# Kernel optimization log

Hardware: AMD Instinct MI355X
Metric: run time of the kernel (lower is better)

The kernel has to match this reference:

```python
import jax, jax.numpy as jnp
import numpy as np

B, TXT_T, MEL_T, N_MEL = 32, 256, 1600, 40
PAD_MAG = 1.0e12


def setup_inputs() -> dict:
    key = jax.random.key(0)
    k1, k2, k3, k4 = jax.random.split(key, 4)
    mu_logvar = jax.random.normal(k1, (B, TXT_T, 2 * N_MEL), jnp.float32)
    z = jax.random.normal(k2, (B, N_MEL, MEL_T), jnp.float32)
    text_lengths = jax.random.randint(k3, (B,), TXT_T // 2, TXT_T + 1).astype(jnp.int32)
    mel_lengths = jax.random.randint(k4, (B,), MEL_T // 2, MEL_T + 1).astype(jnp.int32)
    return {"mu_logvar": mu_logvar, "z": z,
            "text_lengths": text_lengths, "mel_lengths": mel_lengths}


def _mdn_log_prob(mu_logvar, z):
    # mu_logvar: [B, L, 2C], z: [B, C, T] -> log_prob_matrix [B, L, T]
    C = z.shape[1]
    mu, logvar = jnp.split(mu_logvar, 2, axis=-1)          # [B, L, C] each
    invvar = jnp.exp(-logvar)                               # [B, L, C]
    # mean_c((z - mu)^2 * invvar) expanded via matmuls (no [B,L,T,C] tensor)
    t1 = jnp.einsum('bct,blc->blt', z * z, invvar)
    t2 = jnp.einsum('bct,blc->blt', z, mu * invvar)
    t3 = jnp.sum(mu * mu * invvar, axis=-1)[:, :, None]
    mse = t1 - 2.0 * t2 + t3                                # [B, L, T]
    return -0.5 * (mse / C + jnp.mean(logvar, axis=-1)[:, :, None])


def _forward_dp(lp):
    # forward algorithm: log_alpha over (txt position, mel time) via scan over T
    Bb, L, T = lp.shape
    alpha0 = jnp.full((Bb, L + 1), -PAD_MAG, lp.dtype).at[:, 1].set(lp[:, 0, 0])

    def step(alpha, lp_t):
        stay = alpha[:, 1:] + 1e-7
        go = alpha[:, :-1] + 1e-7
        new = jnp.logaddexp(stay, go) + lp_t                # [B, L]
        alpha_new = jnp.concatenate(
            [jnp.full((Bb, 1), -PAD_MAG, lp.dtype), new], axis=1)
        return alpha_new, new

    _, ys = jax.lax.scan(step, alpha0, jnp.moveaxis(lp[:, :, 1:], 2, 0))
    log_alpha = jnp.concatenate([alpha0[:, 1:][None], ys], axis=0)  # [T, B, L]
    return log_alpha


def _viterbi(lp, text_lengths, mel_lengths):
    Bb, L, T = lp.shape
    beta0 = jnp.full((Bb, L), -PAD_MAG, lp.dtype).at[:, 0].set(lp[:, 0, 0])

    def fstep(beta, lp_t):
        shifted = jnp.concatenate(
            [jnp.full((Bb, 1), -PAD_MAG, lp.dtype), beta[:, :-1]], axis=1)
        new = jnp.maximum(beta, shifted) + lp_t
        return new, new

    _, ys = jax.lax.scan(fstep, beta0, jnp.moveaxis(lp[:, :, 1:], 2, 0))
    log_beta = jnp.transpose(jnp.concatenate([beta0[None], ys], axis=0), (1, 2, 0))  # [B, L, T]

    b_idx = jnp.arange(Bb)
    r0 = (text_lengths - 1).astype(jnp.float32)
    c0 = (mel_lengths - 1).astype(jnp.float32)

    def bstep(carry, _):
        rows, cols = carry
        ri = rows.astype(jnp.int32)
        ci = cols.astype(jnp.int32)
        # torch negative indexing wraps -> emulate with mod
        val_go = log_beta[b_idx, (ri - 1) % L, (ci - 1) % T]
        val_stay = log_beta[b_idx, ri % L, (ci - 1) % T]
        is_go = (val_go > val_stay).astype(rows.dtype)
        new_rows = jax.nn.relu(rows - is_go + 1.0) - 1.0
        new_cols = jax.nn.relu(cols) - 1.0
        return (new_rows, new_cols), new_rows

    _, path_ys = jax.lax.scan(bstep, (r0, c0), None, length=T - 1)
    full = jnp.concatenate([r0[None], path_ys], axis=0)     # [T, B], backward order
    path = full[::-1].T                                     # [B, T], chronological
    align = jax.nn.one_hot(path.astype(jnp.int32), L, dtype=lp.dtype)  # [B, T, L]

    def shift(a, ml):
        # F.pad(..., (-pad, pad)) on time axis: shift valid region to the front
        rolled = jnp.roll(a, -(T - ml), axis=0)
        mask = (jnp.arange(T) < ml)[:, None].astype(a.dtype)
        return rolled * mask

    return jax.vmap(shift)(align, mel_lengths)              # [B, T, L]


def reference(mu_logvar, z, text_lengths, mel_lengths):
    lp = _mdn_log_prob(mu_logvar, z)                        # [B, L, T]
    log_alpha = _forward_dp(lp)                             # [T, B, L]
    b_idx = jnp.arange(lp.shape[0])
    alpha_last = log_alpha[mel_lengths - 1, b_idx, text_lengths - 1]
    mdn_loss = -(alpha_last / mel_lengths.astype(alpha_last.dtype))  # [B]
    alignment = _viterbi(lp, text_lengths, mel_lengths)     # [B, T, L]
    return mdn_loss, alignment, lp
```

## Files before the change

### kernel.cpp

```cpp
#include <hip/hip_runtime.h>
#include <cstdint>
#include <math.h>

#define BB   32
#define LLEN 256
#define TLEN 1600
#define NC   40
#define NEGPADF (-1.0e12f)
#define NEGPADD (-1.0e12)

#define OFF_ALIGN 32
#define OFF_LP    (32 + (size_t)BB * TLEN * LLEN)

#define WSB_A    0
#define WSB_KC   (WSB_A + (size_t)BB * LLEN * 80 * 8)
#define WSB_LPT  (WSB_KC + (size_t)BB * LLEN * 8)
#define WSB_PATH (WSB_LPT + (size_t)BB * TLEN * LLEN * 4)

__device__ __forceinline__ int imin(int a, int b) { return a < b ? a : b; }

__device__ __forceinline__ float lsef(float a, float b) {
  a += 1e-7f; b += 1e-7f;
  float m = fmaxf(a, b);
  float d = fabsf(a - b);
  return m + __logf(1.0f + __expf(-d));
}

__global__ __launch_bounds__(256) void prep_kernel(
    const float* __restrict__ mu_logvar, double* __restrict__ A, double* __restrict__ Kc) {
  int row = blockIdx.x * 4 + (threadIdx.x >> 6);
  int lane = threadIdx.x & 63;
  const float* src = mu_logvar + (size_t)row * (2 * NC);
  double mu = 0.0, lv = 0.0, iv = 0.0, part = 0.0;
  if (lane < NC) {
    mu = (double)src[lane];
    lv = (double)src[NC + lane];
    iv = exp(-lv);
    part = mu * mu * iv + lv;
  }
  for (int m = 1; m < 64; m <<= 1) part += __shfl_xor(part, m, 64);
  const double s = -0.5 / (double)NC;
  if (lane < NC) {
    A[(size_t)row * 80 + lane]      = s * iv;
    A[(size_t)row * 80 + NC + lane] = (1.0 / (double)NC) * mu * iv;
  }
  if (lane == 0) Kc[row] = s * part;
}

__global__ __launch_bounds__(128) void lp_kernel(
    const float* __restrict__ z, const double* __restrict__ A,
    const double* __restrict__ Kc, float* __restrict__ out,
    float* __restrict__ lpTh) {
  int b  = blockIdx.z;
  int l0 = blockIdx.y * 32;
  int t0 = blockIdx.x * 128;
  int tid = threadIdx.x;
  int t = t0 + tid;
  int tv = imin(t, TLEN - 1);
  bool act = (t < TLEN);

  float* lp_out = out + OFF_LP;
  float* loS    = out + OFF_ALIGN;

  float zr[NC];
  const float* zb = z + (size_t)b * NC * TLEN;
  #pragma unroll
  for (int c = 0; c < NC; ++c) zr[c] = zb[(size_t)c * TLEN + tv];

  __shared__ __align__(16) double tile[128][33];
  const double* Ab = A + ((size_t)b * LLEN + l0) * 80;
  const double* Kb = Kc + (size_t)b * LLEN + l0;

  #pragma unroll 2
  for (int j = 0; j < 32; ++j) {
    const double* Ar = Ab + (size_t)j * 80;
    double a0 = Kb[j], a1 = 0.0, a2 = 0.0, a3 = 0.0;
    #pragma unroll
    for (int c = 0; c < NC; c += 2) {
      double z0 = (double)zr[c], z1 = (double)zr[c + 1];
      a0 = fma(Ar[c],          z0 * z0, a0);
      a1 = fma(Ar[NC + c],     z0,      a1);
      a2 = fma(Ar[c + 1],      z1 * z1, a2);
      a3 = fma(Ar[NC + c + 1], z1,      a3);
    }
    double accd = (a0 + a2) + (a1 + a3);
    if (act) lp_out[((size_t)b * LLEN + l0 + j) * TLEN + t] = (float)accd;
    tile[tid][j] = accd;
  }
  __syncthreads();
  #pragma unroll
  for (int p = 0; p < 8; ++p) {
    int idx = p * 128 + tid;
    int r = idx >> 3, c4 = idx & 7;
    int tr = t0 + r;
    if (tr < TLEN) {
      float h[4], lo[4];
      #pragma unroll
      for (int i = 0; i < 4; ++i) {
        double d = tile[r][c4 * 4 + i];
        float hh = (float)d;
        h[i] = hh;
        lo[i] = (float)(d - (double)hh);
      }
      size_t base = ((size_t)b * TLEN + tr) * LLEN + l0 + c4 * 4;
      *(float4*)(lpTh + base) = make_float4(h[0], h[1], h[2], h[3]);
      *(float4*)(loS + base)  = make_float4(lo[0], lo[1], lo[2], lo[3]);
    }
  }
}

__global__ __launch_bounds__(64) void dp_kernel(
    const float* __restrict__ lpTh, const float* __restrict__ outR,
    const int* __restrict__ tlen, const int* __restrict__ mlen,
    float* __restrict__ out, int* __restrict__ pathg) {
  int bid = blockIdx.x;
  int lane = threadIdx.x;
  bool is_beta = (bid >= BB);
  int b = is_beta ? bid - BB : bid;
  int tl = tlen[b];
  int ml = mlen[b];
  const float* lpb = lpTh + (size_t)b * TLEN * LLEN;
  const float* lob = outR + OFF_ALIGN + (size_t)b * TLEN * LLEN;
  int rsrc = (lane + 63) & 63;

  if (!is_beta) {
    float4 ring[16];
    #pragma unroll
    for (int k = 0; k < 16; ++k)
      ring[k] = *(const float4*)(lpb + (size_t)imin(1 + k, TLEN - 1) * LLEN + 4 * lane);
    float lp00 = lpb[0];
    float o0 = (lane == 0) ? lp00 : NEGPADF;
    float o1 = NEGPADF, o2 = NEGPADF, o3 = NEGPADF;
    float q = __shfl(o3, rsrc, 64);
    auto step = [&](int t, float4& slot) {
      float4 lp4 = slot;
      slot = *(const float4*)(lpb + (size_t)imin(t + 16, TLEN - 1) * LLEN + 4 * lane);
      float p = (lane == 0) ? NEGPADF : q;
      float n0 = lsef(o0, p)  + lp4.x;
      float n1 = lsef(o1, o0) + lp4.y;
      float n2 = lsef(o2, o1) + lp4.z;
      float n3 = lsef(o3, o2) + lp4.w;
      o0 = n0; o1 = n1; o2 = n2; o3 = n3;
      q = __shfl(o3, rsrc, 64);
    };
    int t = 1;
    for (; t + 15 < ml; t += 16) {
      step(t + 0,  ring[0]);  step(t + 1,  ring[1]);
      step(t + 2,  ring[2]);  step(t + 3,  ring[3]);
      step(t + 4,  ring[4]);  step(t + 5,  ring[5]);
      step(t + 6,  ring[6]);  step(t + 7,  ring[7]);
      step(t + 8,  ring[8]);  step(t + 9,  ring[9]);
      step(t + 10, ring[10]); step(t + 11, ring[11]);
      step(t + 12, ring[12]); step(t + 13, ring[13]);
      step(t + 14, ring[14]); step(t + 15, ring[15]);
    }
    #pragma unroll
    for (int k = 0; k < 16; ++k) { if (t + k < ml) step(t + k, ring[k]); }
    int fr = tl - 1;
    if (lane == (fr >> 2)) {
      int s = fr & 3;
      float val = (s == 0) ? o0 : (s == 1) ? o1 : (s == 2) ? o2 : o3;
      out[b] = -val / (float)ml;
    }
  } else {
    __shared__ uint32_t Dbits[256][TLEN / 32];
    float4 rh[16], rl[16];
    #pragma unroll
    for (int k = 0; k < 16; ++k) {
      size_t off = (size_t)imin(1 + k, TLEN - 1) * LLEN + 4 * lane;
      rh[k] = *(const float4*)(lpb + off);
      rl[k] = *(const float4*)(lob + off);
    }
    double lp00 = (double)lpb[0] + (double)lob[0];
    double o0 = (lane == 0) ? lp00 : NEGPADD;
    double o1 = NEGPADD, o2 = NEGPADD, o3 = NEGPADD;
    double q = __shfl(o3, rsrc, 64);
    uint32_t a0 = 0, a1 = (lane == 0) ? 1u : 0u, a2 = 0, a3 = 0;
    auto step = [&](int t, float4& sh, float4& sl) {
      double l0 = (double)sh.x + (double)sl.x;
      double l1 = (double)sh.y + (double)sl.y;
      double l2 = (double)sh.z + (double)sl.z;
      double l3 = (double)sh.w + (double)sl.w;
      size_t off = (size_t)imin(t + 16, TLEN - 1) * LLEN + 4 * lane;
      sh = *(const float4*)(lpb + off);
      sl = *(const float4*)(lob + off);
      double p = (lane == 0) ? NEGPADD : q;
      double n0 = fmax(o0, p)  + l0;
      double n1 = fmax(o1, o0) + l1;
      double n2 = fmax(o2, o1) + l2;
      double n3 = fmax(o3, o2) + l3;
      q = __shfl(n3, rsrc, 64);
      uint32_t bit = 1u << (t & 31);
      if (q  > n0) a0 |= bit;
      if (n0 > n1) a1 |= bit;
      if (n1 > n2) a2 |= bit;
      if (n2 > n3) a3 |= bit;
      o0 = n0; o1 = n1; o2 = n2; o3 = n3;
      if ((t & 31) == 31) {
        int w = t >> 5;
        Dbits[4 * lane + 0][w] = a0; a0 = 0;
        Dbits[4 * lane + 1][w] = a1; a1 = 0;
        Dbits[4 * lane + 2][w] = a2; a2 = 0;
        Dbits[4 * lane + 3][w] = a3; a3 = 0;
      }
    };
    int t = 1;
    for (; t + 15 < ml; t += 16) {
      step(t + 0,  rh[0],  rl[0]);  step(t + 1,  rh[1],  rl[1]);
      step(t + 2,  rh[2],  rl[2]);  step(t + 3,  rh[3],  rl[3]);
      step(t + 4,  rh[4],  rl[4]);  step(t + 5,  rh[5],  rl[5]);
      step(t + 6,  rh[6],  rl[6]);  step(t + 7,  rh[7],  rl[7]);
      step(t + 8,  rh[8],  rl[8]);  step(t + 9,  rh[9],  rl[9]);
      step(t + 10, rh[10], rl[10]); step(t + 11, rh[11], rl[11]);
      step(t + 12, rh[12], rl[12]); step(t + 13, rh[13], rl[13]);
      step(t + 14, rh[14], rl[14]); step(t + 15, rh[15], rl[15]);
    }
    #pragma unroll
    for (int k = 0; k < 16; ++k) { if (t + k < ml) step(t + k, rh[k], rl[k]); }
    if (((ml - 1) & 31) != 31) {
      int w = (ml - 1) >> 5;
      Dbits[4 * lane + 0][w] = a0;
      Dbits[4 * lane + 1][w] = a1;
      Dbits[4 * lane + 2][w] = a2;
      Dbits[4 * lane + 3][w] = a3;
    }
    __builtin_amdgcn_s_waitcnt(0xC07F);

    if (lane == 0) {
      int* pb = pathg + b * TLEN;
      int r = tl - 1;
      pb[ml - 1] = r;
      int curR = 1 << 30, curW = -1;
      uint32_t W = 0;
      for (int qq = ml - 2; qq >= 0; --qq) {
        int w = qq >> 5;
        if (r >= 0 && (r != curR || w != curW)) { W = Dbits[r][w]; curR = r; curW = w; }
        int g = (r >= 0) ? (int)((W >> (qq & 31)) & 1u) : 0;
        r -= g;
        pb[qq] = r;
      }
    }
  }
}

__global__ __launch_bounds__(256) void zero_kernel(float* __restrict__ out) {
  size_t i = ((size_t)blockIdx.x * 256 + threadIdx.x) * 4;
  *(float4*)(out + OFF_ALIGN + i) = make_float4(0.f, 0.f, 0.f, 0.f);
}

__global__ __launch_bounds__(256) void ones_kernel(
    const int* __restrict__ mlen, const int* __restrict__ pathg, float* __restrict__ out) {
  int b = blockIdx.x;
  int ml = mlen[b];
  float* al = out + OFF_ALIGN;
  for (int t = threadIdx.x; t < ml; t += 256) {
    int p = pathg[b * TLEN + t];
    if (p >= 0) al[((size_t)b * TLEN + t) * LLEN + p] = 1.0f;
  }
}

extern "C" void kernel_launch(void* const* d_in, const int* in_sizes, int n_in,
                              void* d_out, int out_size, void* d_ws, size_t ws_size,
                              hipStream_t stream) {
  const float* mu_logvar = (const float*)d_in[0];
  const float* z         = (const float*)d_in[1];
  const int*   tlv       = (const int*)d_in[2];
  const int*   mlv       = (const int*)d_in[3];
  float* out = (float*)d_out;
  char*  wsb = (char*)d_ws;

  double* Ad   = (double*)(wsb + WSB_A);
  double* Kcd  = (double*)(wsb + WSB_KC);
  float*  lpTh = (float*)(wsb + WSB_LPT);
  int*    path = (int*)(wsb + WSB_PATH);

  prep_kernel<<<dim3(BB * LLEN / 4), 256, 0, stream>>>(mu_logvar, Ad, Kcd);
  lp_kernel<<<dim3(13, 8, BB), 128, 0, stream>>>(z, Ad, Kcd, out, lpTh);
  dp_kernel<<<dim3(2 * BB), 64, 0, stream>>>(lpTh, out, tlv, mlv, out, path);
  zero_kernel<<<dim3((BB * TLEN * LLEN) / (256 * 4)), 256, 0, stream>>>(out);
  ones_kernel<<<dim3(BB), 256, 0, stream>>>(mlv, path, out);
}
```

Before: 588.8 us.

## Add producer wave staging DP inputs via double-buffered LDS; fuse zero+ones kernels

The DP kernel now runs two waves per block. A producer wave loads batches of lp rows from global memory into a double-buffered shared-memory ring and synchronizes with s_barrier, so the consumer wave's serial recurrence only reads from LDS instead of waiting on global loads. The zero-fill and one-hot scatter kernels are merged into a single finalize kernel, which removes a launch and the separate pass. The lp tile-transpose is split into two halves to shrink shared memory. The cost is a barrier on every batch of 8 steps, and the consumer now runs padded iterations past ml, which needs the captured final values and the tail handling of the Dbits words.

```diff
diff --git a/kernel.cpp b/kernel.cpp
--- a/kernel.cpp
+++ b/kernel.cpp
@@ -8,6 +8,7 @@
 #define NC   40
 #define NEGPADF (-1.0e12f)
 #define NEGPADD (-1.0e12)
+#define NBATCH 8
 
 #define OFF_ALIGN 32
 #define OFF_LP    (32 + (size_t)BB * TLEN * LLEN)
@@ -19,11 +20,18 @@
 
 __device__ __forceinline__ int imin(int a, int b) { return a < b ? a : b; }
 
-__device__ __forceinline__ float lsef(float a, float b) {
-  a += 1e-7f; b += 1e-7f;
-  float m = fmaxf(a, b);
-  float d = fabsf(a - b);
-  return m + __logf(1.0f + __expf(-d));
+#define WAIT_LGKM0 0xC07F
+
+__device__ __forceinline__ void bar_prod() {
+  asm volatile("" ::: "memory");
+  __builtin_amdgcn_s_waitcnt(WAIT_LGKM0);
+  __builtin_amdgcn_s_barrier();
+  asm volatile("" ::: "memory");
+}
+__device__ __forceinline__ void bar_cons() {
+  asm volatile("" ::: "memory");
+  __builtin_amdgcn_s_barrier();
+  asm volatile("" ::: "memory");
 }
 
 __global__ __launch_bounds__(256) void prep_kernel(
@@ -67,164 +75,186 @@
   #pragma unroll
   for (int c = 0; c < NC; ++c) zr[c] = zb[(size_t)c * TLEN + tv];
 
-  __shared__ __align__(16) double tile[128][33];
+  __shared__ __align__(16) double tile[128][17];
   const double* Ab = A + ((size_t)b * LLEN + l0) * 80;
   const double* Kb = Kc + (size_t)b * LLEN + l0;
 
-  #pragma unroll 2
-  for (int j = 0; j < 32; ++j) {
-    const double* Ar = Ab + (size_t)j * 80;
-    double a0 = Kb[j], a1 = 0.0, a2 = 0.0, a3 = 0.0;
+  for (int g = 0; g < 2; ++g) {
+    for (int j16 = 0; j16 < 16; ++j16) {
+      int j = g * 16 + j16;
+      const double* Ar = Ab + (size_t)j * 80;
+      double a0 = Kb[j], a1 = 0.0, a2 = 0.0, a3 = 0.0;
+      #pragma unroll
+      for (int c = 0; c < NC; c += 2) {
+        double z0 = (double)zr[c], z1 = (double)zr[c + 1];
+        a0 = fma(Ar[c],          z0 * z0, a0);
+        a1 = fma(Ar[NC + c],     z0,      a1);
+        a2 = fma(Ar[c + 1],      z1 * z1, a2);
+        a3 = fma(Ar[NC + c + 1], z1,      a3);
+      }
+      double accd = (a0 + a2) + (a1 + a3);
+      if (act) lp_out[((size_t)b * LLEN + l0 + j) * TLEN + t] = (float)accd;
+      tile[tid][j16] = accd;
+    }
+    __syncthreads();
     #pragma unroll
-    for (int c = 0; c < NC; c += 2) {
-      double z0 = (double)zr[c], z1 = (double)zr[c + 1];
-      a0 = fma(Ar[c],          z0 * z0, a0);
-      a1 = fma(Ar[NC + c],     z0,      a1);
-      a2 = fma(Ar[c + 1],      z1 * z1, a2);
-      a3 = fma(Ar[NC + c + 1], z1,      a3);
-    }
-    double accd = (a0 + a2) + (a1 + a3);
-    if (act) lp_out[((size_t)b * LLEN + l0 + j) * TLEN + t] = (float)accd;
-    tile[tid][j] = accd;
-  }
-  __syncthreads();
-  #pragma unroll
-  for (int p = 0; p < 8; ++p) {
-    int idx = p * 128 + tid;
-    int r = idx >> 3, c4 = idx & 7;
-    int tr = t0 + r;
-    if (tr < TLEN) {
-      float h[4], lo[4];
-      #pragma unroll
-      for (int i = 0; i < 4; ++i) {
-        double d = tile[r][c4 * 4 + i];
-        float hh = (float)d;
-        h[i] = hh;
-        lo[i] = (float)(d - (double)hh);
-      }
-      size_t base = ((size_t)b * TLEN + tr) * LLEN + l0 + c4 * 4;
-      *(float4*)(lpTh + base) = make_float4(h[0], h[1], h[2], h[3]);
-      *(float4*)(loS + base)  = make_float4(lo[0], lo[1], lo[2], lo[3]);
-    }
-  }
-}
-
-__global__ __launch_bounds__(64) void dp_kernel(
-    const float* __restrict__ lpTh, const float* __restrict__ outR,
+    for (int p = 0; p < 4; ++p) {
+      int idx = p * 128 + tid;
+      int r = idx >> 2, c4 = idx & 3;
+      int tr = t0 + r;
+      if (tr < TLEN) {
+        float h[4], lo[4];
+        #pragma unroll
+        for (int i = 0; i < 4; ++i) {
+          double d = tile[r][c4 * 4 + i];
+          float hh = (float)d;
+          h[i] = hh;
+          lo[i] = (float)(d - (double)hh);
+        }
+        size_t base = ((size_t)b * TLEN + tr) * LLEN + l0 + g * 16 + c4 * 4;
+        *(float4*)(lpTh + base) = make_float4(h[0], h[1], h[2], h[3]);
+        *(float4*)(loS + base)  = make_float4(lo[0], lo[1], lo[2], lo[3]);
+      }
+    }
+    __syncthreads();
+  }
+}
+
+__global__ __launch_bounds__(128, 1) void dp_kernel(
+    const float* __restrict__ lpTh, const float* outR,
     const int* __restrict__ tlen, const int* __restrict__ mlen,
     float* __restrict__ out, int* __restrict__ pathg) {
   int bid = blockIdx.x;
-  int lane = threadIdx.x;
   bool is_beta = (bid >= BB);
   int b = is_beta ? bid - BB : bid;
+  int tid = threadIdx.x;
+  int lane = tid & 63;
+  int wv = tid >> 6;
   int tl = tlen[b];
   int ml = mlen[b];
   const float* lpb = lpTh + (size_t)b * TLEN * LLEN;
   const float* lob = outR + OFF_ALIGN + (size_t)b * TLEN * LLEN;
-  int rsrc = (lane + 63) & 63;
-
-  if (!is_beta) {
-    float4 ring[16];
-    #pragma unroll
-    for (int k = 0; k < 16; ++k)
-      ring[k] = *(const float4*)(lpb + (size_t)imin(1 + k, TLEN - 1) * LLEN + 4 * lane);
+  int nint = (ml - 2 + NBATCH) / NBATCH;
+
+  __shared__ __align__(16) float hbuf[2][NBATCH][LLEN];
+  __shared__ __align__(16) float lbuf[2][NBATCH][LLEN];
+  __shared__ uint32_t Dbits[LLEN][TLEN / 32];
+
+  if (wv == 1) {
+    const float* ph = lpb + 4 * lane;
+    const float* pl = lob + 4 * lane;
+    float4 Ah[NBATCH], Al[NBATCH], Bh[NBATCH], Bl[NBATCH];
+    auto ld_batch = [&](int w, float4* Dh, float4* Dl) {
+      #pragma unroll
+      for (int j = 0; j < NBATCH; ++j) {
+        int c = imin(1 + NBATCH * w + j, TLEN - 1);
+        Dh[j] = *(const float4*)(ph + (size_t)c * LLEN);
+        if (is_beta) Dl[j] = *(const float4*)(pl + (size_t)c * LLEN);
+      }
+    };
+    auto st_batch = [&](int w, float4* Dh, float4* Dl) {
+      int s = w & 1;
+      #pragma unroll
+      for (int j = 0; j < NBATCH; ++j) {
+        *(float4*)(&hbuf[s][j][4 * lane]) = Dh[j];
+        if (is_beta) *(float4*)(&lbuf[s][j][4 * lane]) = Dl[j];
+      }
+    };
+    ld_batch(0, Ah, Al);
+    ld_batch(1, Bh, Bl);
+    for (int w = 0; w < nint; w += 2) {
+      st_batch(w, Ah, Al);
+      bar_prod();
+      ld_batch(w + 2, Ah, Al);
+      if (w + 1 < nint) {
+        st_batch(w + 1, Bh, Bl);
+        bar_prod();
+        ld_batch(w + 3, Bh, Bl);
+      }
+    }
+  } else if (!is_beta) {
+    int rsrc = (lane + 63) & 63;
     float lp00 = lpb[0];
     float o0 = (lane == 0) ? lp00 : NEGPADF;
     float o1 = NEGPADF, o2 = NEGPADF, o3 = NEGPADF;
+    float f0 = o0, f1 = o1, f2 = o2, f3 = o3;
     float q = __shfl(o3, rsrc, 64);
-    auto step = [&](int t, float4& slot) {
-      float4 lp4 = slot;
-      slot = *(const float4*)(lpb + (size_t)imin(t + 16, TLEN - 1) * LLEN + 4 * lane);
-      float p = (lane == 0) ? NEGPADF : q;
-      float n0 = lsef(o0, p)  + lp4.x;
-      float n1 = lsef(o1, o0) + lp4.y;
-      float n2 = lsef(o2, o1) + lp4.z;
-      float n3 = lsef(o3, o2) + lp4.w;
-      o0 = n0; o1 = n1; o2 = n2; o3 = n3;
-      q = __shfl(o3, rsrc, 64);
-    };
     int t = 1;
-    for (; t + 15 < ml; t += 16) {
-      step(t + 0,  ring[0]);  step(t + 1,  ring[1]);
-      step(t + 2,  ring[2]);  step(t + 3,  ring[3]);
-      step(t + 4,  ring[4]);  step(t + 5,  ring[5]);
-      step(t + 6,  ring[6]);  step(t + 7,  ring[7]);
-      step(t + 8,  ring[8]);  step(t + 9,  ring[9]);
-      step(t + 10, ring[10]); step(t + 11, ring[11]);
-      step(t + 12, ring[12]); step(t + 13, ring[13]);
-      step(t + 14, ring[14]); step(t + 15, ring[15]);
-    }
-    #pragma unroll
-    for (int k = 0; k < 16; ++k) { if (t + k < ml) step(t + k, ring[k]); }
+    for (int w = 0; w < nint; ++w) {
+      bar_cons();
+      int s = w & 1;
+      #pragma unroll
+      for (int j = 0; j < NBATCH; ++j, ++t) {
+        float4 lp4 = *(const float4*)(&hbuf[s][j][4 * lane]);
+        float p = (lane == 0) ? NEGPADF : q;
+        float m0 = fmaxf(o0, p),  d0 = fabsf(o0 - p);
+        float m1 = fmaxf(o1, o0), d1 = fabsf(o1 - o0);
+        float m2 = fmaxf(o2, o1), d2 = fabsf(o2 - o1);
+        float m3 = fmaxf(o3, o2), d3 = fabsf(o3 - o2);
+        float n0 = m0 + 1e-7f + __logf(1.0f + __expf(-d0)) + lp4.x;
+        float n1 = m1 + 1e-7f + __logf(1.0f + __expf(-d1)) + lp4.y;
+        float n2 = m2 + 1e-7f + __logf(1.0f + __expf(-d2)) + lp4.z;
+        float n3 = m3 + 1e-7f + __logf(1.0f + __expf(-d3)) + lp4.w;
+        o0 = n0; o1 = n1; o2 = n2; o3 = n3;
+        q = __shfl(o3, rsrc, 64);
+        if (t == ml - 1) { f0 = o0; f1 = o1; f2 = o2; f3 = o3; }
+      }
+    }
     int fr = tl - 1;
     if (lane == (fr >> 2)) {
-      int s = fr & 3;
-      float val = (s == 0) ? o0 : (s == 1) ? o1 : (s == 2) ? o2 : o3;
+      int sx = fr & 3;
+      float val = (sx == 0) ? f0 : (sx == 1) ? f1 : (sx == 2) ? f2 : f3;
       out[b] = -val / (float)ml;
     }
   } else {
-    __shared__ uint32_t Dbits[256][TLEN / 32];
-    float4 rh[16], rl[16];
-    #pragma unroll
-    for (int k = 0; k < 16; ++k) {
-      size_t off = (size_t)imin(1 + k, TLEN - 1) * LLEN + 4 * lane;
-      rh[k] = *(const float4*)(lpb + off);
-      rl[k] = *(const float4*)(lob + off);
-    }
+    int rsrc = (lane + 63) & 63;
     double lp00 = (double)lpb[0] + (double)lob[0];
     double o0 = (lane == 0) ? lp00 : NEGPADD;
     double o1 = NEGPADD, o2 = NEGPADD, o3 = NEGPADD;
+    uint32_t a0 = 0, a1 = (lane == 0) ? 1u : 0u, a2 = 0, a3 = 0;
     double q = __shfl(o3, rsrc, 64);
-    uint32_t a0 = 0, a1 = (lane == 0) ? 1u : 0u, a2 = 0, a3 = 0;
-    auto step = [&](int t, float4& sh, float4& sl) {
-      double l0 = (double)sh.x + (double)sl.x;
-      double l1 = (double)sh.y + (double)sl.y;
-      double l2 = (double)sh.z + (double)sl.z;
-      double l3 = (double)sh.w + (double)sl.w;
-      size_t off = (size_t)imin(t + 16, TLEN - 1) * LLEN + 4 * lane;
-      sh = *(const float4*)(lpb + off);
-      sl = *(const float4*)(lob + off);
-      double p = (lane == 0) ? NEGPADD : q;
-      double n0 = fmax(o0, p)  + l0;
-      double n1 = fmax(o1, o0) + l1;
-      double n2 = fmax(o2, o1) + l2;
-      double n3 = fmax(o3, o2) + l3;
-      q = __shfl(n3, rsrc, 64);
-      uint32_t bit = 1u << (t & 31);
-      if (q  > n0) a0 |= bit;
-      if (n0 > n1) a1 |= bit;
-      if (n1 > n2) a2 |= bit;
-      if (n2 > n3) a3 |= bit;
-      o0 = n0; o1 = n1; o2 = n2; o3 = n3;
-      if ((t & 31) == 31) {
-        int w = t >> 5;
-        Dbits[4 * lane + 0][w] = a0; a0 = 0;
-        Dbits[4 * lane + 1][w] = a1; a1 = 0;
-        Dbits[4 * lane + 2][w] = a2; a2 = 0;
-        Dbits[4 * lane + 3][w] = a3; a3 = 0;
-      }
-    };
     int t = 1;
-    for (; t + 15 < ml; t += 16) {
-      step(t + 0,  rh[0],  rl[0]);  step(t + 1,  rh[1],  rl[1]);
-      step(t + 2,  rh[2],  rl[2]);  step(t + 3,  rh[3],  rl[3]);
-      step(t + 4,  rh[4],  rl[4]);  step(t + 5,  rh[5],  rl[5]);
-      step(t + 6,  rh[6],  rl[6]);  step(t + 7,  rh[7],  rl[7]);
-      step(t + 8,  rh[8],  rl[8]);  step(t + 9,  rh[9],  rl[9]);
-      step(t + 10, rh[10], rl[10]); step(t + 11, rh[11], rl[11]);
-      step(t + 12, rh[12], rl[12]); step(t + 13, rh[13], rl[13]);
-      step(t + 14, rh[14], rl[14]); step(t + 15, rh[15], rl[15]);
-    }
-    #pragma unroll
-    for (int k = 0; k < 16; ++k) { if (t + k < ml) step(t + k, rh[k], rl[k]); }
-    if (((ml - 1) & 31) != 31) {
-      int w = (ml - 1) >> 5;
-      Dbits[4 * lane + 0][w] = a0;
-      Dbits[4 * lane + 1][w] = a1;
-      Dbits[4 * lane + 2][w] = a2;
-      Dbits[4 * lane + 3][w] = a3;
-    }
-    __builtin_amdgcn_s_waitcnt(0xC07F);
+    for (int w = 0; w < nint; ++w) {
+      bar_cons();
+      int s = w & 1;
+      #pragma unroll
+      for (int j = 0; j < NBATCH; ++j, ++t) {
+        float4 h4 = *(const float4*)(&hbuf[s][j][4 * lane]);
+        float4 l4 = *(const float4*)(&lbuf[s][j][4 * lane]);
+        double l0 = (double)h4.x + (double)l4.x;
+        double l1 = (double)h4.y + (double)l4.y;
+        double l2 = (double)h4.z + (double)l4.z;
+        double l3 = (double)h4.w + (double)l4.w;
+        double p = (lane == 0) ? NEGPADD : q;
+        double n0 = fmax(o0, p)  + l0;
+        double n1 = fmax(o1, o0) + l1;
+        double n2 = fmax(o2, o1) + l2;
+        double n3 = fmax(o3, o2) + l3;
+        q = __shfl(n3, rsrc, 64);
+        uint32_t bit = 1u << (t & 31);
+        if (q  > n0) a0 |= bit;
+        if (n0 > n1) a1 |= bit;
+        if (n1 > n2) a2 |= bit;
+        if (n2 > n3) a3 |= bit;
+        o0 = n0; o1 = n1; o2 = n2; o3 = n3;
+        if ((t & 31) == 31) {
+          int wd = t >> 5;
+          Dbits[4 * lane + 0][wd] = a0; a0 = 0;
+          Dbits[4 * lane + 1][wd] = a1; a1 = 0;
+          Dbits[4 * lane + 2][wd] = a2; a2 = 0;
+          Dbits[4 * lane + 3][wd] = a3; a3 = 0;
+        }
+      }
+    }
+    int tend = nint * NBATCH;
+    if ((tend & 31) != 31) {
+      int wd = tend >> 5;
+      Dbits[4 * lane + 0][wd] = a0;
+      Dbits[4 * lane + 1][wd] = a1;
+      Dbits[4 * lane + 2][wd] = a2;
+      Dbits[4 * lane + 3][wd] = a3;
+    }
+    __builtin_amdgcn_s_waitcnt(WAIT_LGKM0);
 
     if (lane == 0) {
       int* pb = pathg + b * TLEN;
@@ -233,8 +263,8 @@
       int curR = 1 << 30, curW = -1;
       uint32_t W = 0;
       for (int qq = ml - 2; qq >= 0; --qq) {
-        int w = qq >> 5;
-        if (r >= 0 && (r != curR || w != curW)) { W = Dbits[r][w]; curR = r; curW = w; }
+        int wd = qq >> 5;
+        if (r >= 0 && (r != curR || wd != curW)) { W = Dbits[r][wd]; curR = r; curW = wd; }
         int g = (r >= 0) ? (int)((W >> (qq & 31)) & 1u) : 0;
         r -= g;
         pb[qq] = r;
@@ -243,19 +273,27 @@
   }
 }
 
-__global__ __launch_bounds__(256) void zero_kernel(float* __restrict__ out) {
-  size_t i = ((size_t)blockIdx.x * 256 + threadIdx.x) * 4;
-  *(float4*)(out + OFF_ALIGN + i) = make_float4(0.f, 0.f, 0.f, 0.f);
-}
-
-__global__ __launch_bounds__(256) void ones_kernel(
-    const int* __restrict__ mlen, const int* __restrict__ pathg, float* __restrict__ out) {
-  int b = blockIdx.x;
-  int ml = mlen[b];
-  float* al = out + OFF_ALIGN;
-  for (int t = threadIdx.x; t < ml; t += 256) {
-    int p = pathg[b * TLEN + t];
-    if (p >= 0) al[((size_t)b * TLEN + t) * LLEN + p] = 1.0f;
+__global__ __launch_bounds__(256) void finalize_kernel(
+    const int* __restrict__ mlen, const int* __restrict__ pathg,
+    float* __restrict__ out) {
+  int b = blockIdx.y;
+  int t0 = blockIdx.x * 8;
+  float* al = out + OFF_ALIGN + (size_t)b * TLEN * LLEN;
+  float4 z4 = make_float4(0.f, 0.f, 0.f, 0.f);
+  #pragma unroll
+  for (int p = 0; p < 2; ++p) {
+    int idx = p * 256 + threadIdx.x;
+    int r = idx >> 6, c4 = idx & 63;
+    *(float4*)(al + (size_t)(t0 + r) * LLEN + c4 * 4) = z4;
+  }
+  __syncthreads();
+  if (threadIdx.x < 8) {
+    int t = t0 + threadIdx.x;
+    int ml = mlen[b];
+    if (t < ml) {
+      int p = pathg[b * TLEN + t];
+      if (p >= 0) al[(size_t)t * LLEN + p] = 1.0f;
+    }
   }
 }
 
@@ -276,7 +314,6 @@
 
   prep_kernel<<<dim3(BB * LLEN / 4), 256, 0, stream>>>(mu_logvar, Ad, Kcd);
   lp_kernel<<<dim3(13, 8, BB), 128, 0, stream>>>(z, Ad, Kcd, out, lpTh);
-  dp_kernel<<<dim3(2 * BB), 64, 0, stream>>>(lpTh, out, tlv, mlv, out, path);
-  zero_kernel<<<dim3((BB * TLEN * LLEN) / (256 * 4)), 256, 0, stream>>>(out);
-  ones_kernel<<<dim3(BB), 256, 0, stream>>>(mlv, path, out);
-}
+  dp_kernel<<<dim3(2 * BB), 128, 0, stream>>>(lpTh, out, tlv, mlv, out, path);
+  finalize_kernel<<<dim3(TLEN / 8, BB), 256, 0, stream>>>(mlv, path, out);
+}
```

New measurement: 1.002 ms. 1.7x slower.
